# Kernel tuning notes

Measured on AMD Instinct MI355X. Metric: run time of the kernel, lower is better.

Reference implementation:

```python
import jax, jax.numpy as jnp
import numpy as np

B, T, I, H = 64, 1024, 256, 256


def setup_inputs() -> dict:
    key = jax.random.key(0)
    ks = jax.random.split(key, 7)
    s_in = 1.0 / np.sqrt(I)
    s_h = 1.0 / np.sqrt(H)
    return {
        "x": jax.random.normal(ks[0], (B, T, I), dtype=jnp.float32),
        "W_ih0": jax.random.normal(ks[1], (H, I), dtype=jnp.float32) * s_in,
        "b_ih0": jax.random.normal(ks[2], (H,), dtype=jnp.float32) * s_in,
        "W_hh0": jax.random.normal(ks[3], (H, H), dtype=jnp.float32) * s_h,
        "W_ih1": jax.random.normal(ks[4], (H, H), dtype=jnp.float32) * s_h,
        "b_ih1": jax.random.normal(ks[5], (H,), dtype=jnp.float32) * s_h,
        "W_hh1": jax.random.normal(ks[6], (H, H), dtype=jnp.float32) * s_h,
    }


def _elman_layer(x, W_ih, b_ih, W_hh):
    # Batch the input projection across all timesteps (the fusion the torch
    # loop misses), then scan only the sequential hidden update.
    xp = jnp.einsum("bti,hi->bth", x, W_ih) + b_ih  # [B,T,H]
    h0 = jnp.zeros((x.shape[0], W_hh.shape[0]), dtype=x.dtype)

    def step(h, xt):  # xt: [B,H]
        h = jnp.tanh(xt + h @ W_hh.T)
        return h, h

    _, ys = jax.lax.scan(step, h0, jnp.swapaxes(xp, 0, 1))  # [T,B,H]
    return jnp.swapaxes(ys, 0, 1)  # [B,T,H]


def reference(x, W_ih0, b_ih0, W_hh0, W_ih1, b_ih1, W_hh1):
    h = _elman_layer(x, W_ih0, b_ih0, W_hh0)
    h = _elman_layer(h, W_ih1, b_ih1, W_hh1)
    return h
```

## Files before the change

kernel.cpp:

```cpp
#include <hip/hip_runtime.h>
#include <cstdint>


#define HDIM 256
#define TLEN 1024
#define BATCH 64
#define HQ 68

__global__ __launch_bounds__(256) void proj_gemm(
    const float* __restrict__ X,
    const float* __restrict__ W,
    const float* __restrict__ bias,
    float* __restrict__ C, int M)
{
    __shared__ __align__(16) float Ast[16][136];
    __shared__ __align__(16) float Bst[16][68];

    const int tid = threadIdx.x;
    const int tx  = tid & 15;
    const int ty  = tid >> 4;
    const int m0  = blockIdx.x * 128;
    const int n0  = blockIdx.y * 64;

    float acc[8][4];
#pragma unroll
    for (int i = 0; i < 8; ++i)
#pragma unroll
        for (int j = 0; j < 4; ++j) acc[i][j] = 0.f;

    const int ar = tid >> 1;
    const int ah = (tid & 1) * 8;
    const int bn = tid >> 2;
    const int bg = (tid & 3) * 4;

    for (int kc = 0; kc < 16; ++kc) {
        const int k0 = kc * 16;
        const float4 av0 = *reinterpret_cast<const float4*>(&X[(size_t)(m0 + ar) * HDIM + k0 + ah]);
        const float4 av1 = *reinterpret_cast<const float4*>(&X[(size_t)(m0 + ar) * HDIM + k0 + ah + 4]);
        const float4 bv  = *reinterpret_cast<const float4*>(&W[(size_t)(n0 + bn) * HDIM + k0 + bg]);
        __syncthreads();
        Ast[ah + 0][ar] = av0.x; Ast[ah + 1][ar] = av0.y;
        Ast[ah + 2][ar] = av0.z; Ast[ah + 3][ar] = av0.w;
        Ast[ah + 4][ar] = av1.x; Ast[ah + 5][ar] = av1.y;
        Ast[ah + 6][ar] = av1.z; Ast[ah + 7][ar] = av1.w;
        Bst[bg + 0][bn] = bv.x;  Bst[bg + 1][bn] = bv.y;
        Bst[bg + 2][bn] = bv.z;  Bst[bg + 3][bn] = bv.w;
        __syncthreads();
#pragma unroll
        for (int kk = 0; kk < 16; ++kk) {
            const float4 a0 = *reinterpret_cast<const float4*>(&Ast[kk][ty * 8]);
            const float4 a1 = *reinterpret_cast<const float4*>(&Ast[kk][ty * 8 + 4]);
            const float4 b4 = *reinterpret_cast<const float4*>(&Bst[kk][tx * 4]);
            const float av[8] = {a0.x, a0.y, a0.z, a0.w, a1.x, a1.y, a1.z, a1.w};
            const float bb[4] = {b4.x, b4.y, b4.z, b4.w};
#pragma unroll
            for (int i = 0; i < 8; ++i)
#pragma unroll
                for (int j = 0; j < 4; ++j)
                    acc[i][j] = fmaf(av[i], bb[j], acc[i][j]);
        }
    }

    const float4 bias4 = *reinterpret_cast<const float4*>(&bias[n0 + tx * 4]);
    const float bb[4] = {bias4.x, bias4.y, bias4.z, bias4.w};
#pragma unroll
    for (int i = 0; i < 8; ++i) {
        float4 o;
        o.x = acc[i][0] + bb[0];
        o.y = acc[i][1] + bb[1];
        o.z = acc[i][2] + bb[2];
        o.w = acc[i][3] + bb[3];
        *reinterpret_cast<float4*>(&C[(size_t)(m0 + ty * 8 + i) * HDIM + n0 + tx * 4]) = o;
    }
}

__device__ __forceinline__ float fast_tanh(float x)
{
    const float xc = fminf(fmaxf(x, -15.f), 15.f);
    const float e  = __expf(2.f * xc);
    return (e - 1.f) / (e + 1.f);
}

#define PIN4(V) asm volatile("" : "+v"((V).x), "+v"((V).y), "+v"((V).z), "+v"((V).w))

#define STEP4(WC, IDX, SACC)                                                  \
    {                                                                         \
        const float4 hh = *reinterpret_cast<const float4*>(hb + (IDX) * 4);   \
        SACC = fmaf((WC).x, hh.x, SACC); SACC = fmaf((WC).y, hh.y, SACC);     \
        SACC = fmaf((WC).z, hh.z, SACC); SACC = fmaf((WC).w, hh.w, SACC);     \
    }

__global__ __launch_bounds__(1024, 4) void elman_scan(
    const float* __restrict__ xp,
    const float* __restrict__ Whh,
    float* __restrict__ y,
    int T)
{
    const int b    = blockIdx.x;
    const int tid  = threadIdx.x;
    const int lane = tid & 63;
    const int wave = tid >> 6;
    const int j    = wave * 16 + (lane >> 2);
    const int q    = lane & 3;

    const float4* wp = reinterpret_cast<const float4*>(Whh + (size_t)j * HDIM + q * 64);
    float4 w0 = wp[0],  w1 = wp[1],  w2 = wp[2],  w3 = wp[3];
    float4 w4 = wp[4],  w5 = wp[5],  w6 = wp[6],  w7 = wp[7];
    float4 w8 = wp[8],  w9 = wp[9],  w10 = wp[10], w11 = wp[11];
    float4 w12 = wp[12], w13 = wp[13], w14 = wp[14], w15 = wp[15];
    PIN4(w0);  PIN4(w1);  PIN4(w2);  PIN4(w3);
    PIN4(w4);  PIN4(w5);  PIN4(w6);  PIN4(w7);
    PIN4(w8);  PIN4(w9);  PIN4(w10); PIN4(w11);
    PIN4(w12); PIN4(w13); PIN4(w14); PIN4(w15);

    __shared__ __align__(16) float hbuf[2][4 * HQ];

    const float* xrow = xp + (size_t)b * T * HDIM;
    float*       yrow = y  + (size_t)b * T * HDIM;

    const int hpos = (j >> 6) * HQ + (j & 63);
    if (q == 0) hbuf[0][hpos] = 0.f;

    float xv[4];
#pragma unroll
    for (int p = 0; p < 4; ++p) xv[p] = xrow[(size_t)p * HDIM + j];

    __syncthreads();

    int cur = 0;
    for (int t = 0; t < T; t += 4) {
#pragma unroll
        for (int p = 0; p < 4; ++p) {
            int tf = t + p + 4; tf = (tf < T) ? tf : (T - 1);
            const float xnew = xrow[(size_t)tf * HDIM + j];

            const float* hb = &hbuf[cur][q * HQ];
            float s0 = 0.f, s1 = 0.f, s2 = 0.f, s3 = 0.f;

            STEP4(w0, 0, s0);  STEP4(w1, 1, s1);
            STEP4(w2, 2, s2);  STEP4(w3, 3, s3);
            STEP4(w4, 4, s0);  STEP4(w5, 5, s1);
            STEP4(w6, 6, s2);  STEP4(w7, 7, s3);
            __builtin_amdgcn_sched_barrier(0);
            STEP4(w8, 8, s0);   STEP4(w9, 9, s1);
            STEP4(w10, 10, s2); STEP4(w11, 11, s3);
            STEP4(w12, 12, s0); STEP4(w13, 13, s1);
            STEP4(w14, 14, s2); STEP4(w15, 15, s3);

            float s = (s0 + s1) + (s2 + s3);

            s += __shfl_xor(s, 1);
            s += __shfl_xor(s, 2);

            const float hn = fast_tanh(s + xv[p]);

            if (q == 0)      hbuf[cur ^ 1][hpos] = hn;
            else if (q == 1) yrow[(size_t)(t + p) * HDIM + j] = hn;

            xv[p] = xnew;
            cur ^= 1;
            __syncthreads();
        }
    }
}

extern "C" void kernel_launch(void* const* d_in, const int* in_sizes, int n_in,
                              void* d_out, int out_size, void* d_ws, size_t ws_size,
                              hipStream_t stream)
{
    const float* x     = (const float*)d_in[0];
    const float* W_ih0 = (const float*)d_in[1];
    const float* b_ih0 = (const float*)d_in[2];
    const float* W_hh0 = (const float*)d_in[3];
    const float* W_ih1 = (const float*)d_in[4];
    const float* b_ih1 = (const float*)d_in[5];
    const float* W_hh1 = (const float*)d_in[6];

    float* out = (float*)d_out;
    float* xp  = (float*)d_ws;

    const int M = BATCH * TLEN;
    dim3 ggrid(M / 128, HDIM / 64);

    proj_gemm<<<ggrid, 256, 0, stream>>>(x,   W_ih0, b_ih0, xp, M);
    elman_scan<<<BATCH, 1024, 0, stream>>>(xp, W_hh0, out, TLEN);
    proj_gemm<<<ggrid, 256, 0, stream>>>(out, W_ih1, b_ih1, xp, M);
    elman_scan<<<BATCH, 1024, 0, stream>>>(xp, W_hh1, out, TLEN);
}
```

Before: 1.895 ms.

## Split each hidden unit across two threads instead of four in scan kernel

The recurrent scan now uses 512 threads per block, with two lanes per hidden unit each holding 128 weights in registers, instead of 1024 threads with four lanes holding 64 each. This halves the barrier participants and removes one cross-lane shuffle per step, which targets the sync- and latency-bound critical path of the sequential update. In exchange, each thread does twice the FMAs and needs about twice the weight registers, which raises register pressure. The padded shared-memory layout for the hidden state is dropped in favor of a plain 256-float buffer.

```diff
diff --git a/kernel.cpp b/kernel.cpp
--- a/kernel.cpp
+++ b/kernel.cpp
@@ -5,7 +5,6 @@
 #define HDIM 256
 #define TLEN 1024
 #define BATCH 64
-#define HQ 68
 
 __global__ __launch_bounds__(256) void proj_gemm(
     const float* __restrict__ X,
@@ -90,36 +89,41 @@
         SACC = fmaf((WC).z, hh.z, SACC); SACC = fmaf((WC).w, hh.w, SACC);     \
     }
 
-__global__ __launch_bounds__(1024, 4) void elman_scan(
+__global__ __launch_bounds__(512) void elman_scan(
     const float* __restrict__ xp,
     const float* __restrict__ Whh,
     float* __restrict__ y,
     int T)
 {
-    const int b    = blockIdx.x;
-    const int tid  = threadIdx.x;
-    const int lane = tid & 63;
-    const int wave = tid >> 6;
-    const int j    = wave * 16 + (lane >> 2);
-    const int q    = lane & 3;
+    const int b   = blockIdx.x;
+    const int tid = threadIdx.x;
+    const int j   = tid >> 1;
+    const int q   = tid & 1;
 
-    const float4* wp = reinterpret_cast<const float4*>(Whh + (size_t)j * HDIM + q * 64);
-    float4 w0 = wp[0],  w1 = wp[1],  w2 = wp[2],  w3 = wp[3];
-    float4 w4 = wp[4],  w5 = wp[5],  w6 = wp[6],  w7 = wp[7];
-    float4 w8 = wp[8],  w9 = wp[9],  w10 = wp[10], w11 = wp[11];
+    const float4* wp = reinterpret_cast<const float4*>(Whh + (size_t)j * HDIM + q * 128);
+    float4 w0  = wp[0],  w1  = wp[1],  w2  = wp[2],  w3  = wp[3];
+    float4 w4  = wp[4],  w5  = wp[5],  w6  = wp[6],  w7  = wp[7];
+    float4 w8  = wp[8],  w9  = wp[9],  w10 = wp[10], w11 = wp[11];
     float4 w12 = wp[12], w13 = wp[13], w14 = wp[14], w15 = wp[15];
+    float4 w16 = wp[16], w17 = wp[17], w18 = wp[18], w19 = wp[19];
+    float4 w20 = wp[20], w21 = wp[21], w22 = wp[22], w23 = wp[23];
+    float4 w24 = wp[24], w25 = wp[25], w26 = wp[26], w27 = wp[27];
+    float4 w28 = wp[28], w29 = wp[29], w30 = wp[30], w31 = wp[31];
     PIN4(w0);  PIN4(w1);  PIN4(w2);  PIN4(w3);
     PIN4(w4);  PIN4(w5);  PIN4(w6);  PIN4(w7);
     PIN4(w8);  PIN4(w9);  PIN4(w10); PIN4(w11);
     PIN4(w12); PIN4(w13); PIN4(w14); PIN4(w15);
+    PIN4(w16); PIN4(w17); PIN4(w18); PIN4(w19);
+    PIN4(w20); PIN4(w21); PIN4(w22); PIN4(w23);
+    PIN4(w24); PIN4(w25); PIN4(w26); PIN4(w27);
+    PIN4(w28); PIN4(w29); PIN4(w30); PIN4(w31);
 
-    __shared__ __align__(16) float hbuf[2][4 * HQ];
+    __shared__ __align__(16) float hbuf[2][HDIM];
 
     const float* xrow = xp + (size_t)b * T * HDIM;
     float*       yrow = y  + (size_t)b * T * HDIM;
 
-    const int hpos = (j >> 6) * HQ + (j & 63);
-    if (q == 0) hbuf[0][hpos] = 0.f;
+    if (q == 0) hbuf[0][j] = 0.f;
 
     float xv[4];
 #pragma unroll
@@ -134,28 +138,34 @@
             int tf = t + p + 4; tf = (tf < T) ? tf : (T - 1);
             const float xnew = xrow[(size_t)tf * HDIM + j];
 
-            const float* hb = &hbuf[cur][q * HQ];
+            const float* hb = &hbuf[cur][q * 128];
             float s0 = 0.f, s1 = 0.f, s2 = 0.f, s3 = 0.f;
 
-            STEP4(w0, 0, s0);  STEP4(w1, 1, s1);
-            STEP4(w2, 2, s2);  STEP4(w3, 3, s3);
-            STEP4(w4, 4, s0);  STEP4(w5, 5, s1);
-            STEP4(w6, 6, s2);  STEP4(w7, 7, s3);
-            __builtin_amdgcn_sched_barrier(0);
-            STEP4(w8, 8, s0);   STEP4(w9, 9, s1);
+            STEP4(w0,  0,  s0); STEP4(w1,  1,  s1);
+            STEP4(w2,  2,  s2); STEP4(w3,  3,  s3);
+            STEP4(w4,  4,  s0); STEP4(w5,  5,  s1);
+            STEP4(w6,  6,  s2); STEP4(w7,  7,  s3);
+            STEP4(w8,  8,  s0); STEP4(w9,  9,  s1);
             STEP4(w10, 10, s2); STEP4(w11, 11, s3);
             STEP4(w12, 12, s0); STEP4(w13, 13, s1);
             STEP4(w14, 14, s2); STEP4(w15, 15, s3);
+            __builtin_amdgcn_sched_barrier(0);
+            STEP4(w16, 16, s0); STEP4(w17, 17, s1);
+            STEP4(w18, 18, s2); STEP4(w19, 19, s3);
+            STEP4(w20, 20, s0); STEP4(w21, 21, s1);
+            STEP4(w22, 22, s2); STEP4(w23, 23, s3);
+            STEP4(w24, 24, s0); STEP4(w25, 25, s1);
+            STEP4(w26, 26, s2); STEP4(w27, 27, s3);
+            STEP4(w28, 28, s0); STEP4(w29, 29, s1);
+            STEP4(w30, 30, s2); STEP4(w31, 31, s3);
 
             float s = (s0 + s1) + (s2 + s3);
-
             s += __shfl_xor(s, 1);
-            s += __shfl_xor(s, 2);
 
             const float hn = fast_tanh(s + xv[p]);
 
-            if (q == 0)      hbuf[cur ^ 1][hpos] = hn;
-            else if (q == 1) yrow[(size_t)(t + p) * HDIM + j] = hn;
+            if (q == 0) hbuf[cur ^ 1][j] = hn;
+            else        yrow[(size_t)(t + p) * HDIM + j] = hn;
 
             xv[p] = xnew;
             cur ^= 1;
@@ -183,7 +193,7 @@
     dim3 ggrid(M / 128, HDIM / 64);
 
     proj_gemm<<<ggrid, 256, 0, stream>>>(x,   W_ih0, b_ih0, xp, M);
-    elman_scan<<<BATCH, 1024, 0, stream>>>(xp, W_hh0, out, TLEN);
+    elman_scan<<<BATCH, 512, 0, stream>>>(xp, W_hh0, out, TLEN);
     proj_gemm<<<ggrid, 256, 0, stream>>>(out, W_ih1, b_ih1, xp, M);
-    elman_scan<<<BATCH, 1024, 0, stream>>>(xp, W_hh1, out, TLEN);
+    elman_scan<<<BATCH, 512, 0, stream>>>(xp, W_hh1, out, TLEN);
 }
```

After: 2.425 ms. +28.0%, slower.
